# Optimization experiments

Measured on AMD Instinct MI355X. Metric: run time of the kernel, lower is better.

The kernel has to match this reference:

```python
import jax, jax.numpy as jnp
import numpy as np

B, S, D, H = 2, 2048, 1024, 16
DK = D // H  # 64
THETA = 10000.0


def _rope_tables(seq_len, d_k, theta):
    pos = jnp.arange(seq_len, dtype=jnp.float32)  # [S]
    dim = jnp.arange(0, d_k, 2, dtype=jnp.float32)  # [DK/2]
    inv_freq = 1.0 / theta ** (dim / d_k)
    angle = pos[:, None] * inv_freq[None, :]  # [S, DK/2]
    angle = jnp.repeat(angle, 2, axis=-1)  # repeat_interleave -> [S, DK]
    return jnp.cos(angle), jnp.sin(angle)


def _apply_rope(x, cos, sin):
    # x: [..., S, DK]; interleaved pair rotation
    x1 = x[..., ::2]
    x2 = x[..., 1::2]
    x_perm = jnp.stack([-x2, x1], axis=-1).reshape(x.shape)
    return x * cos + x_perm * sin


def setup_inputs() -> dict:
    key = jax.random.key(0)
    ks = jax.random.split(key, 5)
    std = np.sqrt(2.0 / (D + D)).astype(np.float32)
    return {
        "x": jax.random.normal(ks[0], (B, S, D), dtype=jnp.float32),
        "Wq": jax.random.normal(ks[1], (D, D), dtype=jnp.float32) * std,
        "Wk": jax.random.normal(ks[2], (D, D), dtype=jnp.float32) * std,
        "Wv": jax.random.normal(ks[3], (D, D), dtype=jnp.float32) * std,
        "Wo": jax.random.normal(ks[4], (D, D), dtype=jnp.float32) * std,
    }


def reference(x, Wq, Wk, Wv, Wo):
    seq_len = x.shape[-2]
    # projections: weight is [d_out, d_in], applied as x @ W^T
    def split_heads(t):
        return t.reshape(*t.shape[:-1], H, DK).swapaxes(-3, -2)  # [B, H, S, DK]

    Q = split_heads(jnp.einsum('bsd,od->bso', x, Wq))
    K = split_heads(jnp.einsum('bsd,od->bso', x, Wk))
    V = split_heads(jnp.einsum('bsd,od->bso', x, Wv))

    cos, sin = _rope_tables(seq_len, DK, THETA)  # [S, DK]
    Q = _apply_rope(Q, cos, sin)
    K = _apply_rope(K, cos, sin)

    scale = 1.0 / np.sqrt(DK).astype(np.float32)
    logits = jnp.einsum('bhnd,bhmd->bhnm', Q, K) * scale  # [B, H, S, S]
    causal = jnp.tril(jnp.ones((seq_len, seq_len), dtype=bool))
    logits = jnp.where(causal, logits, -jnp.inf)
    probs = jax.nn.softmax(logits, axis=-1)
    attn = jnp.einsum('bhnm,bhmd->bhnd', probs, V)  # [B, H, S, DK]
    attn = attn.swapaxes(-3, -2).reshape(*x.shape[:-1], D)  # [B, S, D]
    return jnp.einsum('bsd,od->bso', attn, Wo)
```

## Files before the change

### kernel.cpp

```cpp
#include <hip/hip_runtime.h>
#include <hip/hip_bf16.h>
#include <cstdint>
#include <cstddef>

#define BB 2
#define SS 2048
#define DD 1024
#define HH 16
#define DKK 64
#define MM (BB*SS)

typedef __bf16 bf16x8 __attribute__((ext_vector_type(8)));
typedef float  f32x4  __attribute__((ext_vector_type(4)));

__device__ __forceinline__ unsigned short f2bf(float f) {
    unsigned u = __float_as_uint(f);
    u += 0x7FFF + ((u >> 16) & 1);
    return (unsigned short)(u >> 16);
}

#if __has_builtin(__builtin_amdgcn_cvt_pk_bf16_f32)
typedef __bf16 bf16v2 __attribute__((ext_vector_type(2)));
__device__ __forceinline__ unsigned pk_bf16(float a, float b) {
    bf16v2 v = __builtin_amdgcn_cvt_pk_bf16_f32(a, b);
    return __builtin_bit_cast(unsigned, v);
}
#else
__device__ __forceinline__ unsigned pk_bf16(float a, float b) {
    return (unsigned)f2bf(a) | ((unsigned)f2bf(b) << 16);
}
#endif

__device__ __forceinline__ void gld_lds16(const void* g, void* l) {
    __builtin_amdgcn_global_load_lds(
        (const __attribute__((address_space(1))) unsigned int*)g,
        (__attribute__((address_space(3))) unsigned int*)l, 16, 0, 0);
}

#define WAIT_VM8() __builtin_amdgcn_s_waitcnt(0x0F78)
#define WAIT_VM4() __builtin_amdgcn_s_waitcnt(0x0F74)
#define WAIT_VM3() __builtin_amdgcn_s_waitcnt(0x0F73)
#define WAIT_VM0() __builtin_amdgcn_s_waitcnt(0x0F70)
#define BARRIER()  __builtin_amdgcn_s_barrier()

__global__ __launch_bounds__(256) void cast_all(const float* __restrict__ x,
                                                const float* __restrict__ wq,
                                                const float* __restrict__ wk,
                                                const float* __restrict__ wv,
                                                const float* __restrict__ wo,
                                                unsigned short* __restrict__ xb,
                                                unsigned short* __restrict__ wb,
                                                float2* __restrict__ tab) {
    const int bid = blockIdx.x;
    if (bid >= 8192) {
        int e = (bid - 8192) * 256 + threadIdx.x;
        int s = e >> 5, dk2 = e & 31;
        float inv_freq = exp2f(-(float)dk2 * 0.4152410118609203f);
        float sn, cs;
        __sincosf((float)s * inv_freq, &sn, &cs);
        tab[e] = make_float2(cs, sn);
        return;
    }
    int i = (bid * 256 + threadIdx.x) * 4;
    const float* src;
    unsigned short* dst;
    if (i < MM * DD) { src = x + i; dst = xb + i; }
    else {
        int e = i - MM * DD;
        int r = e >> 20;
        const float* s0 = (r == 0) ? wq : (r == 1) ? wk : (r == 2) ? wv : wo;
        src = s0 + (e & ((1 << 20) - 1));
        dst = wb + e;
    }
    float4 v = *reinterpret_cast<const float4*>(src);
    ushort4 o;
    o.x = f2bf(v.x); o.y = f2bf(v.y); o.z = f2bf(v.z); o.w = f2bf(v.w);
    *reinterpret_cast<ushort4*>(dst) = o;
}

__global__ __launch_bounds__(256, 3) void gemm_qkv(const unsigned short* __restrict__ A,
                                                   const unsigned short* __restrict__ W,
                                                   const float2* __restrict__ tab,
                                                   unsigned short* __restrict__ Qo,
                                                   unsigned short* __restrict__ Ko,
                                                   unsigned short* __restrict__ Vto) {
    __shared__ __align__(16) unsigned short A0[128 * 32], W0[128 * 32];
    __shared__ __align__(16) unsigned short A1[128 * 32], W1[128 * 32];
    const int tid  = threadIdx.x;
    const int wave = tid >> 6, lane = tid & 63;
    const int quad = lane >> 4, l16 = lane & 15;
    const int wm = wave >> 1, wn = wave & 1;
    const int m0 = blockIdx.y * 128, n0 = blockIdx.x * 128;
    const int sw3 = l16 & 3;

    f32x4 acc[4][4];
    for (int i = 0; i < 4; i++)
        for (int j = 0; j < 4; j++) acc[i][j] = f32x4{0.f, 0.f, 0.f, 0.f};

    auto stage = [&](int k0, unsigned short* As, unsigned short* Ws) {
        for (int c = tid; c < 512; c += 256) {
            int row = c >> 2, g = c & 3;
            int gc = ((g ^ (row & 3)) << 3);
            gld_lds16(A + (size_t)(m0 + row) * DD + k0 + gc, As + c * 8);
            gld_lds16(W + (size_t)(n0 + row) * DD + k0 + gc, Ws + c * 8);
        }
    };
    auto compute = [&](const unsigned short* As, const unsigned short* Ws) {
        bf16x8 af[4], bfb[4];
        for (int i = 0; i < 4; i++)
            af[i] = *reinterpret_cast<const bf16x8*>(As + (wm * 64 + i * 16 + l16) * 32 + ((quad ^ sw3) << 3));
        for (int j = 0; j < 4; j++)
            bfb[j] = *reinterpret_cast<const bf16x8*>(Ws + (wn * 64 + j * 16 + l16) * 32 + ((quad ^ sw3) << 3));
        for (int i = 0; i < 4; i++)
            for (int j = 0; j < 4; j++)
                acc[i][j] = __builtin_amdgcn_mfma_f32_16x16x32_bf16(af[i], bfb[j], acc[i][j], 0, 0, 0);
    };

    stage(0, A0, W0);
    int k0 = 0;
    while (true) {
        BARRIER();
        if (k0 + 32 < DD) { stage(k0 + 32, A1, W1); WAIT_VM4(); } else WAIT_VM0();
        BARRIER();
        compute(A0, W0);
        k0 += 32; if (k0 >= DD) break;

        BARRIER();
        if (k0 + 32 < DD) { stage(k0 + 32, A0, W0); WAIT_VM4(); } else WAIT_VM0();
        BARRIER();
        compute(A1, W1);
        k0 += 32; if (k0 >= DD) break;
    }

    const int region = n0 >> 10;
    if (region < 2) {
        unsigned short* Co = region ? Ko : Qo;
        const float osc = (region == 0) ? 0.18033688011112042f : 1.0f;
        for (int i = 0; i < 4; i++) {
            int mrow = m0 + wm * 64 + i * 16 + quad * 4;
            int b = mrow >> 11, s0 = mrow & 2047;
            for (int j = 0; j < 4; j++) {
                int nc = (n0 + wn * 64 + j * 16 + l16) & 1023;
                int h = nc >> 6, dk = nc & 63;
                const float2* tb = tab + ((size_t)s0 << 5) + (dk >> 1);
                for (int r = 0; r < 4; r++) {
                    float v = acc[i][j][r];
                    float partner = __shfl_xor(v, 1, 64);
                    float2 cs = tb[(size_t)r << 5];
                    float outv = (v * cs.x + ((dk & 1) ? partner : -partner) * cs.y) * osc;
                    Co[((size_t)(b * HH + h) * SS + (s0 + r)) * DKK + dk] = f2bf(outv);
                }
            }
        }
    } else {
        __syncthreads();
        unsigned short* T = A0 + wave * 1024;
        const int dkl = lane >> 2, s4 = (lane & 3) * 4;
        for (int i = 0; i < 4; i++) {
            int ms0 = m0 + wm * 64 + i * 16;
            for (int j = 0; j < 4; j++) {
                int nc0 = n0 + wn * 64 + j * 16;
                for (int r = 0; r < 4; r++)
                    T[(quad * 4 + r) * 17 + l16] = f2bf(acc[i][j][r]);
                ushort4 o;
                o.x = T[(s4 + 0) * 17 + dkl];
                o.y = T[(s4 + 1) * 17 + dkl];
                o.z = T[(s4 + 2) * 17 + dkl];
                o.w = T[(s4 + 3) * 17 + dkl];
                int nc = (nc0 + dkl) & 1023;
                int h = nc >> 6, dk = nc & 63;
                int m = ms0 + s4;
                int b = m >> 11, s = m & 2047;
                *reinterpret_cast<ushort4*>(Vto + ((size_t)((b * HH + h) * DKK + dk)) * SS + s) = o;
            }
        }
    }
}

__global__ __launch_bounds__(256, 3) void gemm_out(const unsigned short* __restrict__ A,
                                                   const unsigned short* __restrict__ W,
                                                   float* __restrict__ C) {
    __shared__ __align__(16) unsigned short A0[64 * 32], W0[128 * 32];
    __shared__ __align__(16) unsigned short A1[64 * 32], W1[128 * 32];
    const int tid  = threadIdx.x;
    const int wave = tid >> 6, lane = tid & 63;
    const int quad = lane >> 4, l16 = lane & 15;
    const int wm = wave >> 1, wn = wave & 1;
    const int m0 = blockIdx.y * 64, n0 = blockIdx.x * 128;
    const int sw3 = l16 & 3;

    f32x4 acc[2][4];
    for (int i = 0; i < 2; i++)
        for (int j = 0; j < 4; j++) acc[i][j] = f32x4{0.f, 0.f, 0.f, 0.f};

    auto stage = [&](int k0, unsigned short* As, unsigned short* Ws) {
        {
            int row = tid >> 2, g = tid & 3;
            int gc = ((g ^ (row & 3)) << 3);
            gld_lds16(A + (size_t)(m0 + row) * DD + k0 + gc, As + tid * 8);
        }
        for (int c = tid; c < 512; c += 256) {
            int row = c >> 2, g = c & 3;
            int gc = ((g ^ (row & 3)) << 3);
            gld_lds16(W + (size_t)(n0 + row) * DD + k0 + gc, Ws + c * 8);
        }
    };
    auto compute = [&](const unsigned short* As, const unsigned short* Ws) {
        bf16x8 af[2], bfb[4];
        for (int i = 0; i < 2; i++)
            af[i] = *reinterpret_cast<const bf16x8*>(As + (wm * 32 + i * 16 + l16) * 32 + ((quad ^ sw3) << 3));
        for (int j = 0; j < 4; j++)
            bfb[j] = *reinterpret_cast<const bf16x8*>(Ws + (wn * 64 + j * 16 + l16) * 32 + ((quad ^ sw3) << 3));
        for (int i = 0; i < 2; i++)
            for (int j = 0; j < 4; j++)
                acc[i][j] = __builtin_amdgcn_mfma_f32_16x16x32_bf16(af[i], bfb[j], acc[i][j], 0, 0, 0);
    };

    stage(0, A0, W0);
    int k0 = 0;
    while (true) {
        BARRIER();
        if (k0 + 32 < DD) { stage(k0 + 32, A1, W1); WAIT_VM3(); } else WAIT_VM0();
        BARRIER();
        compute(A0, W0);
        k0 += 32; if (k0 >= DD) break;

        BARRIER();
        if (k0 + 32 < DD) { stage(k0 + 32, A0, W0); WAIT_VM3(); } else WAIT_VM0();
        BARRIER();
        compute(A1, W1);
        k0 += 32; if (k0 >= DD) break;
    }

    for (int i = 0; i < 2; i++) {
        int mrow = m0 + wm * 32 + i * 16 + quad * 4;
        for (int j = 0; j < 4; j++) {
            int ncol = n0 + wn * 64 + j * 16 + l16;
            for (int r = 0; r < 4; r++)
                C[(size_t)(mrow + r) * DD + ncol] = acc[i][j][r];
        }
    }
}

__global__ __launch_bounds__(256, 3) void attn_kernel(const unsigned short* __restrict__ Qb,
                                                      const unsigned short* __restrict__ Kb,
                                                      const unsigned short* __restrict__ Vtb,
                                                      unsigned short* __restrict__ attn) {
    __shared__ unsigned short K0s[64 * 64], V0s[64 * 64];
    __shared__ unsigned short K1s[64 * 64], V1s[64 * 64];
    __shared__ unsigned short Ps[4][16 * 72];

    const int tid  = threadIdx.x;
    const int wave = tid >> 6, lane = tid & 63;
    const int quad = lane >> 4, l16 = lane & 15;

    const int lin = blockIdx.x;
    const int xcd = lin & 7, idx = lin >> 3;
    const int bh  = xcd * 4 + (idx & 3);
    const int tau = 31 - (idx >> 2);
    const int nST = tau + 1;

    const int swK = l16 & 7;
    const int q0r = tau * 64;

    const unsigned short* Qg = Qb  + (size_t)bh * SS * DKK;
    const unsigned short* Kg = Kb  + (size_t)bh * SS * DKK;
    const unsigned short* Vg = Vtb + (size_t)bh * DKK * SS;

    bf16x8 q0 = *reinterpret_cast<const bf16x8*>(Qg + (size_t)(q0r + wave * 16 + l16) * DKK + quad * 8);
    bf16x8 q1 = *reinterpret_cast<const bf16x8*>(Qg + (size_t)(q0r + wave * 16 + l16) * DKK + 32 + quad * 8);

    bf16x8 vone;
    for (int tt = 0; tt < 8; tt++) vone[tt] = (__bf16)1.0f;

    f32x4 ao[4], al;
    for (int j = 0; j < 4; j++) ao[j] = f32x4{0.f,0.f,0.f,0.f};
    al = f32x4{0.f,0.f,0.f,0.f};

    auto stage = [&](int s, unsigned short* Kd, unsigned short* Vd) {
        const int kv0 = s * 64;
        for (int c = tid; c < 512; c += 256) {
            int rowK = c >> 3, gK = c & 7;
            gld_lds16(Kg + (size_t)(kv0 + rowK) * DKK + ((gK ^ (rowK & 7)) << 3), Kd + c * 8);
            int rowV = c >> 3, gV = c & 7;
            gld_lds16(Vg + (size_t)rowV * SS + kv0 + ((gV ^ (rowV & 7)) << 3), Vd + c * 8);
        }
    };

    auto do_tile = [&](const unsigned short* Kd, const unsigned short* Vd, bool diag) {
        f32x4 sc[4];
        __builtin_amdgcn_s_setprio(1);
        for (int j = 0; j < 4; j++) {
            const unsigned short* kr = Kd + (j * 16 + l16) * 64;
            bf16x8 kf0 = *reinterpret_cast<const bf16x8*>(kr + ((quad ^ swK) << 3));
            bf16x8 kf1 = *reinterpret_cast<const bf16x8*>(kr + (((4 + quad) ^ swK) << 3));
            f32x4 s = f32x4{0.f, 0.f, 0.f, 0.f};
            s = __builtin_amdgcn_mfma_f32_16x16x32_bf16(q0, kf0, s, 0, 0, 0);
            s = __builtin_amdgcn_mfma_f32_16x16x32_bf16(q1, kf1, s, 0, 0, 0);
            sc[j] = s;
        }
        __builtin_amdgcn_s_setprio(0);
        if (diag) {
            for (int j = 0; j < 4; j++) {
                int lcol = j * 16 + l16;
                for (int r = 0; r < 4; r++) {
                    int lrow = wave * 16 + quad * 4 + r;
                    if (lcol > lrow) sc[j][r] = -1e30f;
                }
            }
        }
        for (int j = 0; j < 4; j++)
            for (int r = 0; r < 4; r++)
                sc[j][r] = exp2f(sc[j][r]);

        unsigned short* Pw = Ps[wave];
        for (int r = 0; r < 4; r++) {
            unsigned pA = pk_bf16(sc[0][r], sc[1][r]);
            unsigned pB = pk_bf16(sc[2][r], sc[3][r]);
            int ro = (quad * 4 + r) * 72;
            Pw[ro + l16]      = (unsigned short)pA;
            Pw[ro + 16 + l16] = (unsigned short)(pA >> 16);
            Pw[ro + 32 + l16] = (unsigned short)pB;
            Pw[ro + 48 + l16] = (unsigned short)(pB >> 16);
        }

        __builtin_amdgcn_s_setprio(1);
        for (int ko = 0; ko < 64; ko += 32) {
            bf16x8 pf = *reinterpret_cast<const bf16x8*>(Pw + l16 * 72 + ko + quad * 8);
            al = __builtin_amdgcn_mfma_f32_16x16x32_bf16(pf, vone, al, 0, 0, 0);
            int gg = (ko >> 3) + quad;
            for (int j = 0; j < 4; j++) {
                bf16x8 vf = *reinterpret_cast<const bf16x8*>(Vd + (j * 16 + l16) * 64 + ((gg ^ (l16 & 7)) << 3));
                ao[j] = __builtin_amdgcn_mfma_f32_16x16x32_bf16(pf, vf, ao[j], 0, 0, 0);
            }
        }
        __builtin_amdgcn_s_setprio(0);
    };

    stage(0, K0s, V0s);
    int s = 0;
    while (true) {
        BARRIER();
        if (s + 1 < nST) { stage(s + 1, K1s, V1s); WAIT_VM4(); } else WAIT_VM0();
        BARRIER();
        do_tile(K0s, V0s, s == tau);
        if (++s >= nST) break;

        BARRIER();
        if (s + 1 < nST) { stage(s + 1, K0s, V0s); WAIT_VM4(); } else WAIT_VM0();
        BARRIER();
        do_tile(K1s, V1s, s == tau);
        if (++s >= nST) break;
    }

    const int b = bh >> 4, h = bh & 15;
    for (int r = 0; r < 4; r++) {
        float invL = __builtin_amdgcn_rcpf(al[r]);
        int sr = q0r + wave * 16 + quad * 4 + r;
        for (int j = 0; j < 4; j++)
            attn[((size_t)(b * SS + sr)) * DD + h * DKK + j * 16 + l16] = f2bf(ao[j][r] * invL);
    }
}

extern "C" void kernel_launch(void* const* d_in, const int* in_sizes, int n_in,
                              void* d_out, int out_size, void* d_ws, size_t ws_size,
                              hipStream_t stream) {
    const float* x  = (const float*)d_in[0];
    const float* Wq = (const float*)d_in[1];
    const float* Wk = (const float*)d_in[2];
    const float* Wv = (const float*)d_in[3];
    const float* Wo = (const float*)d_in[4];

    char* ws = (char*)d_ws;
    const size_t MB = 1u << 20;
    unsigned short* xb    = (unsigned short*)(ws);
    unsigned short* wb    = (unsigned short*)(ws + 8  * MB);
    unsigned short* Qbuf  = (unsigned short*)(ws + 16 * MB);
    unsigned short* Kbuf  = (unsigned short*)(ws + 24 * MB);
    unsigned short* Vtbuf = (unsigned short*)(ws + 32 * MB);
    float2*         tab   = (float2*)(ws + 40 * MB);
    unsigned short* attnb = xb;

    cast_all<<<8448, 256, 0, stream>>>(x, Wq, Wk, Wv, Wo, xb, wb, tab);

    gemm_qkv<<<dim3(24, 32), 256, 0, stream>>>(xb, wb, tab, Qbuf, Kbuf, Vtbuf);

    attn_kernel<<<dim3(1024), 256, 0, stream>>>(Qbuf, Kbuf, Vtbuf, attnb);

    gemm_out<<<dim3(8, 64), 256, 0, stream>>>(attnb, wb + 3 * 1024 * 1024, (float*)d_out);
}
```

Measured before the change: 178.7 us.

## Load K/V fragments directly from global memory instead of LDS double-buffering

Removes the shared-memory double-buffered K/V staging and its barriers; each wave now reads its K and V MFMA operands straight from global memory (relying on L1/L2 for reuse across the four waves). Launch bounds rise to 4 blocks per SM since LDS use drops to the P scratch only. This cuts barrier and LDS traffic but quadruples global/L2 requests per block and loses the explicit prefetch overlap, exposing load latency per tile.

```diff
diff --git a/kernel.cpp b/kernel.cpp
--- a/kernel.cpp
+++ b/kernel.cpp
@@ -242,12 +242,10 @@
     }
 }
 
-__global__ __launch_bounds__(256, 3) void attn_kernel(const unsigned short* __restrict__ Qb,
+__global__ __launch_bounds__(256, 4) void attn_kernel(const unsigned short* __restrict__ Qb,
                                                       const unsigned short* __restrict__ Kb,
                                                       const unsigned short* __restrict__ Vtb,
                                                       unsigned short* __restrict__ attn) {
-    __shared__ unsigned short K0s[64 * 64], V0s[64 * 64];
-    __shared__ unsigned short K1s[64 * 64], V1s[64 * 64];
     __shared__ unsigned short Ps[4][16 * 72];
 
     const int tid  = threadIdx.x;
@@ -260,7 +258,6 @@
     const int tau = 31 - (idx >> 2);
     const int nST = tau + 1;
 
-    const int swK = l16 & 7;
     const int q0r = tau * 64;
 
     const unsigned short* Qg = Qb  + (size_t)bh * SS * DKK;
@@ -277,29 +274,34 @@
     for (int j = 0; j < 4; j++) ao[j] = f32x4{0.f,0.f,0.f,0.f};
     al = f32x4{0.f,0.f,0.f,0.f};
 
-    auto stage = [&](int s, unsigned short* Kd, unsigned short* Vd) {
+    const unsigned short* Krow = Kg + (size_t)(l16) * DKK + quad * 8;
+    const unsigned short* Vrow = Vg + (size_t)(l16) * SS + quad * 8;
+
+    for (int s = 0; s < nST; s++) {
         const int kv0 = s * 64;
-        for (int c = tid; c < 512; c += 256) {
-            int rowK = c >> 3, gK = c & 7;
-            gld_lds16(Kg + (size_t)(kv0 + rowK) * DKK + ((gK ^ (rowK & 7)) << 3), Kd + c * 8);
-            int rowV = c >> 3, gV = c & 7;
-            gld_lds16(Vg + (size_t)rowV * SS + kv0 + ((gV ^ (rowV & 7)) << 3), Vd + c * 8);
-        }
-    };
-
-    auto do_tile = [&](const unsigned short* Kd, const unsigned short* Vd, bool diag) {
+        const bool diag = (s == tau);
+
         f32x4 sc[4];
         __builtin_amdgcn_s_setprio(1);
         for (int j = 0; j < 4; j++) {
-            const unsigned short* kr = Kd + (j * 16 + l16) * 64;
-            bf16x8 kf0 = *reinterpret_cast<const bf16x8*>(kr + ((quad ^ swK) << 3));
-            bf16x8 kf1 = *reinterpret_cast<const bf16x8*>(kr + (((4 + quad) ^ swK) << 3));
-            f32x4 s = f32x4{0.f, 0.f, 0.f, 0.f};
-            s = __builtin_amdgcn_mfma_f32_16x16x32_bf16(q0, kf0, s, 0, 0, 0);
-            s = __builtin_amdgcn_mfma_f32_16x16x32_bf16(q1, kf1, s, 0, 0, 0);
-            sc[j] = s;
+            const unsigned short* kr = Krow + (size_t)(kv0 + j * 16) * DKK;
+            bf16x8 kf0 = *reinterpret_cast<const bf16x8*>(kr);
+            bf16x8 kf1 = *reinterpret_cast<const bf16x8*>(kr + 32);
+            f32x4 sa = f32x4{0.f, 0.f, 0.f, 0.f};
+            sa = __builtin_amdgcn_mfma_f32_16x16x32_bf16(q0, kf0, sa, 0, 0, 0);
+            sa = __builtin_amdgcn_mfma_f32_16x16x32_bf16(q1, kf1, sa, 0, 0, 0);
+            sc[j] = sa;
         }
         __builtin_amdgcn_s_setprio(0);
+
+        bf16x8 vf[2][4];
+        #pragma unroll
+        for (int k2 = 0; k2 < 2; k2++)
+            #pragma unroll
+            for (int j = 0; j < 4; j++)
+                vf[k2][j] = *reinterpret_cast<const bf16x8*>(
+                    Vrow + (size_t)(j * 16) * SS + kv0 + k2 * 32);
+
         if (diag) {
             for (int j = 0; j < 4; j++) {
                 int lcol = j * 16 + l16;
@@ -325,32 +327,15 @@
         }
 
         __builtin_amdgcn_s_setprio(1);
-        for (int ko = 0; ko < 64; ko += 32) {
-            bf16x8 pf = *reinterpret_cast<const bf16x8*>(Pw + l16 * 72 + ko + quad * 8);
+        #pragma unroll
+        for (int k2 = 0; k2 < 2; k2++) {
+            bf16x8 pf = *reinterpret_cast<const bf16x8*>(Pw + l16 * 72 + k2 * 32 + quad * 8);
             al = __builtin_amdgcn_mfma_f32_16x16x32_bf16(pf, vone, al, 0, 0, 0);
-            int gg = (ko >> 3) + quad;
-            for (int j = 0; j < 4; j++) {
-                bf16x8 vf = *reinterpret_cast<const bf16x8*>(Vd + (j * 16 + l16) * 64 + ((gg ^ (l16 & 7)) << 3));
-                ao[j] = __builtin_amdgcn_mfma_f32_16x16x32_bf16(pf, vf, ao[j], 0, 0, 0);
-            }
+            #pragma unroll
+            for (int j = 0; j < 4; j++)
+                ao[j] = __builtin_amdgcn_mfma_f32_16x16x32_bf16(pf, vf[k2][j], ao[j], 0, 0, 0);
         }
         __builtin_amdgcn_s_setprio(0);
-    };
-
-    stage(0, K0s, V0s);
-    int s = 0;
-    while (true) {
-        BARRIER();
-        if (s + 1 < nST) { stage(s + 1, K1s, V1s); WAIT_VM4(); } else WAIT_VM0();
-        BARRIER();
-        do_tile(K0s, V0s, s == tau);
-        if (++s >= nST) break;
-
-        BARRIER();
-        if (s + 1 < nST) { stage(s + 1, K0s, V0s); WAIT_VM4(); } else WAIT_VM0();
-        BARRIER();
-        do_tile(K1s, V1s, s == tau);
-        if (++s >= nST) break;
     }
 
     const int b = bh >> 4, h = bh & 15;
```

Result: slower. 281.8 us (+57.7%).
